# Optimization experiments

Hardware: AMD Instinct MI355X
Metric: run time of the kernel (lower is better)

## Reference

```python
import jax, jax.numpy as jnp
import numpy as np

R = 16
ALPHA = 32.0
SCALING = ALPHA / R


def setup_inputs() -> dict:
    key = jax.random.key(0)
    ks = jax.random.split(key, 6)
    B, T, C, O, E = 16, 1500, 1024, 1024, 8
    x = jax.random.normal(ks[0], (B, T, C), dtype=jnp.float32)
    # gate weights per batch element (e.g. softmax-like, but module accepts any)
    w = jax.random.uniform(ks[1], (B, E), dtype=jnp.float32)
    W_base = jax.random.normal(ks[2], (O, C), dtype=jnp.float32) * 0.02
    b_base = jax.random.normal(ks[3], (O,), dtype=jnp.float32) * 0.02
    As = jax.random.normal(ks[4], (E, R, C), dtype=jnp.float32) * 0.02
    Bs = jax.random.normal(ks[5], (E, O, R), dtype=jnp.float32) * 0.02
    return {"x": x, "w": w, "W_base": W_base, "b_base": b_base, "As": As, "Bs": Bs}


def reference(x, w, W_base, b_base, As, Bs):
    # base linear: (B,T,C) @ (C,O) + b
    out = jnp.einsum('btc,oc->bto', x, W_base) + b_base
    # per-expert low-rank: h[b,t,e,r] = x[b,t,:] @ A_e^T
    h = jnp.einsum('btc,erc->bter', x, As)          # (B,T,E,R)
    # y[b,t,e,o] = h @ B_e^T ; gate-weighted sum over experts
    lora = jnp.einsum('bter,eor,be->bto', h, Bs, w)  # (B,T,O)
    return out + lora * SCALING
```

## Files before the change

kernel.cpp:

```cpp
#include <hip/hip_runtime.h>
#include <stdint.h>
#include <stddef.h>


#define B_ 16
#define T_ 1500
#define C_ 1024
#define O_ 1024
#define E_ 8
#define R_ 16
#define ER 128
#define KK 1152
#define BT 24000
#define SCALING 2.0f

typedef __bf16 bf16x8 __attribute__((ext_vector_type(8)));
typedef float f32x4 __attribute__((ext_vector_type(4)));
typedef unsigned short u16;

__device__ inline u16 f2bf(float f) {
  union { float f; unsigned u; } v; v.f = f;
  unsigned u = v.u;
  u += 0x7fff + ((u >> 16) & 1);
  return (u16)(u >> 16);
}

#define GLL(gp, lp)                                                            \
  __builtin_amdgcn_global_load_lds(                                            \
      (const __attribute__((address_space(1))) void*)(gp),                     \
      (__attribute__((address_space(3))) void*)(lp), 16, 0, 0)

__global__ __launch_bounds__(256) void prep_w(const float* __restrict__ Wb,
                                              const float* __restrict__ Bs,
                                              const float* __restrict__ As,
                                              u16* __restrict__ wp,
                                              u16* __restrict__ ap) {
  int idx = blockIdx.x * 256 + threadIdx.x;
  if (idx < O_ * KK) {
    int o = idx / KK;
    int k = idx - o * KK;
    float v;
    if (k < C_) {
      v = Wb[o * C_ + k];
    } else {
      int j = k - C_;
      v = Bs[((j >> 4) * O_ + o) * R_ + (j & 15)];
    }
    wp[idx] = f2bf(v);
  } else {
    int a = idx - O_ * KK;
    ap[a] = f2bf(As[a]);
  }
}

__global__ __launch_bounds__(256) void cvt_h(const float* __restrict__ x,
                                             const u16* __restrict__ ab,
                                             const float* __restrict__ w,
                                             u16* __restrict__ xp) {
  const int mt = blockIdx.x;
  const int tid = threadIdx.x, lane = tid & 63, wv = tid >> 6;
  const int wrow = wv & 1, wcol = wv >> 1, l15 = lane & 15, quad = lane >> 4;
  const int kx = quad ^ (l15 & 3) ^ ((l15 >> 2) & 3);

  __shared__ u16 lA[64 * 40];
  __shared__ u16 lB[128 * 32];

  const size_t row0 = (size_t)mt * 64;

  f32x4 acc[2][4];
#pragma unroll
  for (int i = 0; i < 2; ++i)
#pragma unroll
    for (int j = 0; j < 4; ++j) acc[i][j] = (f32x4){0.f, 0.f, 0.f, 0.f};

  const int idx0 = tid, idx1 = 256 + tid;
  const int r0 = idx0 >> 2, kc0 = (idx0 & 3) ^ (r0 & 3) ^ ((r0 >> 2) & 3);
  const int r1 = idx1 >> 2, kc1 = (idx1 & 3) ^ (r1 & 3) ^ ((r1 >> 2) & 3);

  const int xr0 = tid >> 3;
  const int xr1 = xr0 + 32;
  const int xc = (tid & 7) * 4;

  for (int kt = 0; kt < C_ / 32; ++kt) {
    const int k0 = kt * 32;
    GLL(ab + r0 * C_ + k0 + kc0 * 8, &lB[idx0 * 8]);
    GLL(ab + r1 * C_ + k0 + kc1 * 8, &lB[idx1 * 8]);
    float4 v0 = *(const float4*)&x[(row0 + xr0) * C_ + k0 + xc];
    float4 v1 = *(const float4*)&x[(row0 + xr1) * C_ + k0 + xc];
    ushort4 o0, o1;
    o0.x = f2bf(v0.x); o0.y = f2bf(v0.y); o0.z = f2bf(v0.z); o0.w = f2bf(v0.w);
    o1.x = f2bf(v1.x); o1.y = f2bf(v1.y); o1.z = f2bf(v1.z); o1.w = f2bf(v1.w);
    *(ushort4*)&lA[xr0 * 40 + xc] = o0;
    *(ushort4*)&lA[xr1 * 40 + xc] = o1;
    *(ushort4*)&xp[(row0 + xr0) * KK + k0 + xc] = o0;
    *(ushort4*)&xp[(row0 + xr1) * KK + k0 + xc] = o1;
    __syncthreads();
    bf16x8 af[2], bfr[4];
#pragma unroll
    for (int i = 0; i < 2; ++i)
      af[i] = *(const bf16x8*)&lA[(wrow * 32 + i * 16 + l15) * 40 + quad * 8];
#pragma unroll
    for (int j = 0; j < 4; ++j)
      bfr[j] = *(const bf16x8*)&lB[(wcol * 64 + j * 16 + l15) * 32 + kx * 8];
#pragma unroll
    for (int i = 0; i < 2; ++i)
#pragma unroll
      for (int j = 0; j < 4; ++j)
        acc[i][j] = __builtin_amdgcn_mfma_f32_16x16x32_bf16(af[i], bfr[j], acc[i][j], 0, 0, 0);
    __syncthreads();
  }

#pragma unroll
  for (int j = 0; j < 4; ++j) {
    const int col = wcol * 64 + j * 16 + l15;
    const int e = wcol * 4 + j;
#pragma unroll
    for (int i = 0; i < 2; ++i) {
#pragma unroll
      for (int rr = 0; rr < 4; ++rr) {
        const int row = mt * 64 + wrow * 32 + i * 16 + quad * 4 + rr;
        const int b = row / T_;
        xp[(size_t)row * KK + C_ + col] = f2bf(acc[i][j][rr] * (SCALING * w[b * E_ + e]));
      }
    }
  }
}

__global__ __launch_bounds__(256) void main_gemm(const u16* __restrict__ xp,
                                                 const u16* __restrict__ wp,
                                                 const float* __restrict__ bb,
                                                 float* __restrict__ out) {
  const int id = blockIdx.x;
  const int mt = ((id >> 6) << 3) | (id & 7);
  const int nt = (id >> 3) & 7;
  if (mt >= 188) return;
  const int tid = threadIdx.x, lane = tid & 63, wv = tid >> 6;
  const int wrow = wv & 1, wcol = wv >> 1, l15 = lane & 15, quad = lane >> 4;
  const int kx = quad ^ (l15 & 3) ^ ((l15 >> 2) & 3);

  __shared__ u16 lA[128 * 32];
  __shared__ u16 lB[128 * 32];
  const u16* gA = xp + (size_t)mt * 128 * KK;
  const u16* gB = wp + (size_t)nt * 128 * KK;

  f32x4 acc[4][4];
#pragma unroll
  for (int i = 0; i < 4; ++i)
#pragma unroll
    for (int j = 0; j < 4; ++j) acc[i][j] = (f32x4){0.f, 0.f, 0.f, 0.f};

  const int idx0 = tid, idx1 = 256 + tid;
  const int r0 = idx0 >> 2, kc0 = (idx0 & 3) ^ (r0 & 3) ^ ((r0 >> 2) & 3);
  const int r1 = idx1 >> 2, kc1 = (idx1 & 3) ^ (r1 & 3) ^ ((r1 >> 2) & 3);

  for (int kt = 0; kt < KK / 32; ++kt) {
    const int k0 = kt * 32;
    GLL(gA + (size_t)r0 * KK + k0 + kc0 * 8, &lA[idx0 * 8]);
    GLL(gA + (size_t)r1 * KK + k0 + kc1 * 8, &lA[idx1 * 8]);
    GLL(gB + (size_t)r0 * KK + k0 + kc0 * 8, &lB[idx0 * 8]);
    GLL(gB + (size_t)r1 * KK + k0 + kc1 * 8, &lB[idx1 * 8]);
    __syncthreads();
    bf16x8 af[4], bfr[4];
#pragma unroll
    for (int i = 0; i < 4; ++i) {
      af[i] = *(const bf16x8*)&lA[(wrow * 64 + i * 16 + l15) * 32 + kx * 8];
      bfr[i] = *(const bf16x8*)&lB[(wcol * 64 + i * 16 + l15) * 32 + kx * 8];
    }
#pragma unroll
    for (int i = 0; i < 4; ++i)
#pragma unroll
      for (int j = 0; j < 4; ++j)
        acc[i][j] = __builtin_amdgcn_mfma_f32_16x16x32_bf16(af[i], bfr[j], acc[i][j], 0, 0, 0);
    __syncthreads();
  }

#pragma unroll
  for (int j = 0; j < 4; ++j) {
    const int col = nt * 128 + wcol * 64 + j * 16 + l15;
    const float bias = bb[col];
#pragma unroll
    for (int i = 0; i < 4; ++i) {
#pragma unroll
      for (int rr = 0; rr < 4; ++rr) {
        const int row = mt * 128 + wrow * 64 + i * 16 + quad * 4 + rr;
        if (row < BT) out[(size_t)row * O_ + col] = acc[i][j][rr] + bias;
      }
    }
  }
}

extern "C" void kernel_launch(void* const* d_in, const int* in_sizes, int n_in,
                              void* d_out, int out_size, void* d_ws, size_t ws_size,
                              hipStream_t stream) {
  const float* x = (const float*)d_in[0];
  const float* w = (const float*)d_in[1];
  const float* Wb = (const float*)d_in[2];
  const float* bb = (const float*)d_in[3];
  const float* As = (const float*)d_in[4];
  const float* Bs = (const float*)d_in[5];
  float* out = (float*)d_out;

  u16* xp = (u16*)d_ws;
  u16* wp = xp + (size_t)BT * KK;
  u16* ap = wp + (size_t)O_ * KK;

  prep_w<<<(O_ * KK + ER * C_) / 256, 256, 0, stream>>>(Wb, Bs, As, wp, ap);
  cvt_h<<<375, 256, 0, stream>>>(x, ap, w, xp);
  main_gemm<<<1536, 256, 0, stream>>>(xp, wp, bb, out);
}
```

Measured before the change: 299.0 us.

## Double K-tile depth to 64 and halve cvt_h row tile for more blocks

Both the conversion/low-rank kernel and the main GEMM now stage 64-wide K tiles in LDS with an 8-way XOR swizzle, halving the number of barrier pairs per K loop. cvt_h also processes 32 rows per block instead of 64, doubling its grid to 750 blocks for better occupancy of the memory-bound x conversion pass. The cost is larger LDS footprint per block (32KB in main_gemm), which may reduce concurrent blocks per CU.

```diff
diff --git a/kernel.cpp b/kernel.cpp
--- a/kernel.cpp
+++ b/kernel.cpp
@@ -60,53 +60,55 @@
   const int mt = blockIdx.x;
   const int tid = threadIdx.x, lane = tid & 63, wv = tid >> 6;
   const int wrow = wv & 1, wcol = wv >> 1, l15 = lane & 15, quad = lane >> 4;
-  const int kx = quad ^ (l15 & 3) ^ ((l15 >> 2) & 3);
-
-  __shared__ u16 lA[64 * 40];
-  __shared__ u16 lB[128 * 32];
-
-  const size_t row0 = (size_t)mt * 64;
-
-  f32x4 acc[2][4];
-#pragma unroll
-  for (int i = 0; i < 2; ++i)
-#pragma unroll
-    for (int j = 0; j < 4; ++j) acc[i][j] = (f32x4){0.f, 0.f, 0.f, 0.f};
-
-  const int idx0 = tid, idx1 = 256 + tid;
-  const int r0 = idx0 >> 2, kc0 = (idx0 & 3) ^ (r0 & 3) ^ ((r0 >> 2) & 3);
-  const int r1 = idx1 >> 2, kc1 = (idx1 & 3) ^ (r1 & 3) ^ ((r1 >> 2) & 3);
-
-  const int xr0 = tid >> 3;
-  const int xr1 = xr0 + 32;
+  const int s7 = l15 & 7;
+
+  __shared__ u16 lA[32 * 72];
+  __shared__ u16 lB[128 * 64];
+
+  const size_t row0 = (size_t)mt * 32;
+
+  f32x4 acc[4];
+#pragma unroll
+  for (int j = 0; j < 4; ++j) acc[j] = (f32x4){0.f, 0.f, 0.f, 0.f};
+
+  int brow[4], bko[4];
+#pragma unroll
+  for (int c = 0; c < 4; ++c) {
+    int idx = c * 256 + tid;
+    brow[c] = idx >> 3;
+    bko[c] = (((idx & 7) ^ (brow[c] & 7)) << 3);
+  }
+
+  const int xr = tid >> 3;
   const int xc = (tid & 7) * 4;
 
-  for (int kt = 0; kt < C_ / 32; ++kt) {
-    const int k0 = kt * 32;
-    GLL(ab + r0 * C_ + k0 + kc0 * 8, &lB[idx0 * 8]);
-    GLL(ab + r1 * C_ + k0 + kc1 * 8, &lB[idx1 * 8]);
-    float4 v0 = *(const float4*)&x[(row0 + xr0) * C_ + k0 + xc];
-    float4 v1 = *(const float4*)&x[(row0 + xr1) * C_ + k0 + xc];
+  for (int kt = 0; kt < C_ / 64; ++kt) {
+    const int k0 = kt * 64;
+#pragma unroll
+    for (int c = 0; c < 4; ++c)
+      GLL(ab + brow[c] * C_ + k0 + bko[c], &lB[(c * 256 + tid) * 8]);
+    float4 v0 = *(const float4*)&x[(row0 + xr) * C_ + k0 + xc];
+    float4 v1 = *(const float4*)&x[(row0 + xr) * C_ + k0 + 32 + xc];
     ushort4 o0, o1;
     o0.x = f2bf(v0.x); o0.y = f2bf(v0.y); o0.z = f2bf(v0.z); o0.w = f2bf(v0.w);
     o1.x = f2bf(v1.x); o1.y = f2bf(v1.y); o1.z = f2bf(v1.z); o1.w = f2bf(v1.w);
-    *(ushort4*)&lA[xr0 * 40 + xc] = o0;
-    *(ushort4*)&lA[xr1 * 40 + xc] = o1;
-    *(ushort4*)&xp[(row0 + xr0) * KK + k0 + xc] = o0;
-    *(ushort4*)&xp[(row0 + xr1) * KK + k0 + xc] = o1;
-    __syncthreads();
-    bf16x8 af[2], bfr[4];
-#pragma unroll
-    for (int i = 0; i < 2; ++i)
-      af[i] = *(const bf16x8*)&lA[(wrow * 32 + i * 16 + l15) * 40 + quad * 8];
-#pragma unroll
-    for (int j = 0; j < 4; ++j)
-      bfr[j] = *(const bf16x8*)&lB[(wcol * 64 + j * 16 + l15) * 32 + kx * 8];
-#pragma unroll
-    for (int i = 0; i < 2; ++i)
+    *(ushort4*)&lA[xr * 72 + xc] = o0;
+    *(ushort4*)&lA[xr * 72 + 32 + xc] = o1;
+    *(ushort4*)&xp[(row0 + xr) * KK + k0 + xc] = o0;
+    *(ushort4*)&xp[(row0 + xr) * KK + k0 + 32 + xc] = o1;
+    __syncthreads();
+#pragma unroll
+    for (int kk = 0; kk < 2; ++kk) {
+      bf16x8 af = *(const bf16x8*)&lA[(wrow * 16 + l15) * 72 + kk * 32 + quad * 8];
+      bf16x8 bfr[4];
 #pragma unroll
       for (int j = 0; j < 4; ++j)
-        acc[i][j] = __builtin_amdgcn_mfma_f32_16x16x32_bf16(af[i], bfr[j], acc[i][j], 0, 0, 0);
+        bfr[j] = *(const bf16x8*)&lB[(wcol * 64 + j * 16 + l15) * 64 +
+                                     (((kk * 4 + quad) ^ s7) << 3)];
+#pragma unroll
+      for (int j = 0; j < 4; ++j)
+        acc[j] = __builtin_amdgcn_mfma_f32_16x16x32_bf16(af, bfr[j], acc[j], 0, 0, 0);
+    }
     __syncthreads();
   }
 
@@ -115,13 +117,10 @@
     const int col = wcol * 64 + j * 16 + l15;
     const int e = wcol * 4 + j;
 #pragma unroll
-    for (int i = 0; i < 2; ++i) {
-#pragma unroll
-      for (int rr = 0; rr < 4; ++rr) {
-        const int row = mt * 64 + wrow * 32 + i * 16 + quad * 4 + rr;
-        const int b = row / T_;
-        xp[(size_t)row * KK + C_ + col] = f2bf(acc[i][j][rr] * (SCALING * w[b * E_ + e]));
-      }
+    for (int rr = 0; rr < 4; ++rr) {
+      const int row = mt * 32 + wrow * 16 + quad * 4 + rr;
+      const int b = row / T_;
+      xp[(size_t)row * KK + C_ + col] = f2bf(acc[j][rr] * (SCALING * w[b * E_ + e]));
     }
   }
 }
@@ -136,10 +135,10 @@
   if (mt >= 188) return;
   const int tid = threadIdx.x, lane = tid & 63, wv = tid >> 6;
   const int wrow = wv & 1, wcol = wv >> 1, l15 = lane & 15, quad = lane >> 4;
-  const int kx = quad ^ (l15 & 3) ^ ((l15 >> 2) & 3);
-
-  __shared__ u16 lA[128 * 32];
-  __shared__ u16 lB[128 * 32];
+  const int s7 = l15 & 7;
+
+  __shared__ u16 lA[128 * 64];
+  __shared__ u16 lB[128 * 64];
   const u16* gA = xp + (size_t)mt * 128 * KK;
   const u16* gB = wp + (size_t)nt * 128 * KK;
 
@@ -149,28 +148,38 @@
 #pragma unroll
     for (int j = 0; j < 4; ++j) acc[i][j] = (f32x4){0.f, 0.f, 0.f, 0.f};
 
-  const int idx0 = tid, idx1 = 256 + tid;
-  const int r0 = idx0 >> 2, kc0 = (idx0 & 3) ^ (r0 & 3) ^ ((r0 >> 2) & 3);
-  const int r1 = idx1 >> 2, kc1 = (idx1 & 3) ^ (r1 & 3) ^ ((r1 >> 2) & 3);
-
-  for (int kt = 0; kt < KK / 32; ++kt) {
-    const int k0 = kt * 32;
-    GLL(gA + (size_t)r0 * KK + k0 + kc0 * 8, &lA[idx0 * 8]);
-    GLL(gA + (size_t)r1 * KK + k0 + kc1 * 8, &lA[idx1 * 8]);
-    GLL(gB + (size_t)r0 * KK + k0 + kc0 * 8, &lB[idx0 * 8]);
-    GLL(gB + (size_t)r1 * KK + k0 + kc1 * 8, &lB[idx1 * 8]);
-    __syncthreads();
-    bf16x8 af[4], bfr[4];
-#pragma unroll
-    for (int i = 0; i < 4; ++i) {
-      af[i] = *(const bf16x8*)&lA[(wrow * 64 + i * 16 + l15) * 32 + kx * 8];
-      bfr[i] = *(const bf16x8*)&lB[(wcol * 64 + i * 16 + l15) * 32 + kx * 8];
-    }
-#pragma unroll
-    for (int i = 0; i < 4; ++i)
-#pragma unroll
-      for (int j = 0; j < 4; ++j)
-        acc[i][j] = __builtin_amdgcn_mfma_f32_16x16x32_bf16(af[i], bfr[j], acc[i][j], 0, 0, 0);
+  int srow[4], sko[4];
+#pragma unroll
+  for (int c = 0; c < 4; ++c) {
+    int idx = c * 256 + tid;
+    srow[c] = idx >> 3;
+    sko[c] = (((idx & 7) ^ (srow[c] & 7)) << 3);
+  }
+
+  for (int kt = 0; kt < KK / 64; ++kt) {
+    const int k0 = kt * 64;
+#pragma unroll
+    for (int c = 0; c < 4; ++c)
+      GLL(gA + (size_t)srow[c] * KK + k0 + sko[c], &lA[(c * 256 + tid) * 8]);
+#pragma unroll
+    for (int c = 0; c < 4; ++c)
+      GLL(gB + (size_t)srow[c] * KK + k0 + sko[c], &lB[(c * 256 + tid) * 8]);
+    __syncthreads();
+#pragma unroll
+    for (int kk = 0; kk < 2; ++kk) {
+      bf16x8 af[4], bfr[4];
+#pragma unroll
+      for (int i = 0; i < 4; ++i) {
+        const int ko = (((kk * 4 + quad) ^ s7) << 3);
+        af[i] = *(const bf16x8*)&lA[(wrow * 64 + i * 16 + l15) * 64 + ko];
+        bfr[i] = *(const bf16x8*)&lB[(wcol * 64 + i * 16 + l15) * 64 + ko];
+      }
+#pragma unroll
+      for (int i = 0; i < 4; ++i)
+#pragma unroll
+        for (int j = 0; j < 4; ++j)
+          acc[i][j] = __builtin_amdgcn_mfma_f32_16x16x32_bf16(af[i], bfr[j], acc[i][j], 0, 0, 0);
+    }
     __syncthreads();
   }
 
@@ -205,6 +214,6 @@
   u16* ap = wp + (size_t)O_ * KK;
 
   prep_w<<<(O_ * KK + ER * C_) / 256, 256, 0, stream>>>(Wb, Bs, As, wp, ap);
-  cvt_h<<<375, 256, 0, stream>>>(x, ap, w, xp);
+  cvt_h<<<750, 256, 0, stream>>>(x, ap, w, xp);
   main_gemm<<<1536, 256, 0, stream>>>(xp, wp, bb, out);
 }
```

Result: faster. 285.7 us (-4.4%).

## Split x conversion into a streaming kernel and retile the LoRA-h GEMM

Applied to the files above, without the earlier changes.

The fused convert-plus-h-GEMM kernel becomes two kernels. The first is a fully parallel fp32-to-bf16 conversion of x into the workspace. The second is an h GEMM that reads the bf16 x with direct global-to-LDS loads, uses a 64-wide K tile and an XOR swizzle. The goal is to stop the fp32 load and convert work from serialising with the MFMA loop across only 375 blocks. The cost is an extra launch and a second read of x in bf16 from the workspace.

```diff
diff --git a/kernel.cpp b/kernel.cpp
--- a/kernel.cpp
+++ b/kernel.cpp
@@ -17,6 +17,7 @@
 typedef __bf16 bf16x8 __attribute__((ext_vector_type(8)));
 typedef float f32x4 __attribute__((ext_vector_type(4)));
 typedef unsigned short u16;
+typedef u16 u16x8 __attribute__((ext_vector_type(8)));
 
 __device__ inline u16 f2bf(float f) {
   union { float f; unsigned u; } v; v.f = f;
@@ -53,19 +54,36 @@
   }
 }
 
-__global__ __launch_bounds__(256) void cvt_h(const float* __restrict__ x,
-                                             const u16* __restrict__ ab,
-                                             const float* __restrict__ w,
-                                             u16* __restrict__ xp) {
+__global__ __launch_bounds__(256) void cvt(const float* __restrict__ x,
+                                           u16* __restrict__ xp) {
+  const int t0 = blockIdx.x * 256 + threadIdx.x;
+#pragma unroll
+  for (int u = 0; u < 6; ++u) {
+    const int chunk = u * 512000 + t0;
+    const int row = chunk >> 7;
+    const int cc = (chunk & 127) * 8;
+    const float4 v0 = *(const float4*)&x[(size_t)row * C_ + cc];
+    const float4 v1 = *(const float4*)&x[(size_t)row * C_ + cc + 4];
+    u16x8 o;
+    o[0] = f2bf(v0.x); o[1] = f2bf(v0.y); o[2] = f2bf(v0.z); o[3] = f2bf(v0.w);
+    o[4] = f2bf(v1.x); o[5] = f2bf(v1.y); o[6] = f2bf(v1.z); o[7] = f2bf(v1.w);
+    *(u16x8*)&xp[(size_t)row * KK + cc] = o;
+  }
+}
+
+__global__ __launch_bounds__(256) void h_gemm(const u16* __restrict__ xp,
+                                              const u16* __restrict__ ab,
+                                              const float* __restrict__ w,
+                                              u16* __restrict__ xpo) {
   const int mt = blockIdx.x;
   const int tid = threadIdx.x, lane = tid & 63, wv = tid >> 6;
   const int wrow = wv & 1, wcol = wv >> 1, l15 = lane & 15, quad = lane >> 4;
-  const int kx = quad ^ (l15 & 3) ^ ((l15 >> 2) & 3);
-
-  __shared__ u16 lA[64 * 40];
-  __shared__ u16 lB[128 * 32];
-
-  const size_t row0 = (size_t)mt * 64;
+  const int s7 = l15 & 7;
+
+  __shared__ u16 lA[64 * 64];
+  __shared__ u16 lB[128 * 64];
+
+  const u16* gA = xp + (size_t)mt * 64 * KK;
 
   f32x4 acc[2][4];
 #pragma unroll
@@ -73,40 +91,45 @@
 #pragma unroll
     for (int j = 0; j < 4; ++j) acc[i][j] = (f32x4){0.f, 0.f, 0.f, 0.f};
 
-  const int idx0 = tid, idx1 = 256 + tid;
-  const int r0 = idx0 >> 2, kc0 = (idx0 & 3) ^ (r0 & 3) ^ ((r0 >> 2) & 3);
-  const int r1 = idx1 >> 2, kc1 = (idx1 & 3) ^ (r1 & 3) ^ ((r1 >> 2) & 3);
-
-  const int xr0 = tid >> 3;
-  const int xr1 = xr0 + 32;
-  const int xc = (tid & 7) * 4;
-
-  for (int kt = 0; kt < C_ / 32; ++kt) {
-    const int k0 = kt * 32;
-    GLL(ab + r0 * C_ + k0 + kc0 * 8, &lB[idx0 * 8]);
-    GLL(ab + r1 * C_ + k0 + kc1 * 8, &lB[idx1 * 8]);
-    float4 v0 = *(const float4*)&x[(row0 + xr0) * C_ + k0 + xc];
-    float4 v1 = *(const float4*)&x[(row0 + xr1) * C_ + k0 + xc];
-    ushort4 o0, o1;
-    o0.x = f2bf(v0.x); o0.y = f2bf(v0.y); o0.z = f2bf(v0.z); o0.w = f2bf(v0.w);
-    o1.x = f2bf(v1.x); o1.y = f2bf(v1.y); o1.z = f2bf(v1.z); o1.w = f2bf(v1.w);
-    *(ushort4*)&lA[xr0 * 40 + xc] = o0;
-    *(ushort4*)&lA[xr1 * 40 + xc] = o1;
-    *(ushort4*)&xp[(row0 + xr0) * KK + k0 + xc] = o0;
-    *(ushort4*)&xp[(row0 + xr1) * KK + k0 + xc] = o1;
-    __syncthreads();
-    bf16x8 af[2], bfr[4];
-#pragma unroll
-    for (int i = 0; i < 2; ++i)
-      af[i] = *(const bf16x8*)&lA[(wrow * 32 + i * 16 + l15) * 40 + quad * 8];
-#pragma unroll
-    for (int j = 0; j < 4; ++j)
-      bfr[j] = *(const bf16x8*)&lB[(wcol * 64 + j * 16 + l15) * 32 + kx * 8];
-#pragma unroll
-    for (int i = 0; i < 2; ++i)
+  int arow[2], ako[2], brow[4], bko[4];
+#pragma unroll
+  for (int c = 0; c < 2; ++c) {
+    int idx = c * 256 + tid;
+    arow[c] = idx >> 3;
+    ako[c] = (((idx & 7) ^ (arow[c] & 7)) << 3);
+  }
+#pragma unroll
+  for (int c = 0; c < 4; ++c) {
+    int idx = c * 256 + tid;
+    brow[c] = idx >> 3;
+    bko[c] = (((idx & 7) ^ (brow[c] & 7)) << 3);
+  }
+
+  for (int kt = 0; kt < C_ / 64; ++kt) {
+    const int k0 = kt * 64;
+#pragma unroll
+    for (int c = 0; c < 2; ++c)
+      GLL(gA + (size_t)arow[c] * KK + k0 + ako[c], &lA[(c * 256 + tid) * 8]);
+#pragma unroll
+    for (int c = 0; c < 4; ++c)
+      GLL(ab + brow[c] * C_ + k0 + bko[c], &lB[(c * 256 + tid) * 8]);
+    __syncthreads();
+#pragma unroll
+    for (int kk = 0; kk < 2; ++kk) {
+      const int ko = (((kk * 4 + quad) ^ s7) << 3);
+      bf16x8 af[2], bfr[4];
+#pragma unroll
+      for (int i = 0; i < 2; ++i)
+        af[i] = *(const bf16x8*)&lA[(wrow * 32 + i * 16 + l15) * 64 + ko];
 #pragma unroll
       for (int j = 0; j < 4; ++j)
-        acc[i][j] = __builtin_amdgcn_mfma_f32_16x16x32_bf16(af[i], bfr[j], acc[i][j], 0, 0, 0);
+        bfr[j] = *(const bf16x8*)&lB[(wcol * 64 + j * 16 + l15) * 64 + ko];
+#pragma unroll
+      for (int i = 0; i < 2; ++i)
+#pragma unroll
+        for (int j = 0; j < 4; ++j)
+          acc[i][j] = __builtin_amdgcn_mfma_f32_16x16x32_bf16(af[i], bfr[j], acc[i][j], 0, 0, 0);
+    }
     __syncthreads();
   }
 
@@ -120,7 +143,7 @@
       for (int rr = 0; rr < 4; ++rr) {
         const int row = mt * 64 + wrow * 32 + i * 16 + quad * 4 + rr;
         const int b = row / T_;
-        xp[(size_t)row * KK + C_ + col] = f2bf(acc[i][j][rr] * (SCALING * w[b * E_ + e]));
+        xpo[(size_t)row * KK + C_ + col] = f2bf(acc[i][j][rr] * (SCALING * w[b * E_ + e]));
       }
     }
   }
@@ -205,6 +228,7 @@
   u16* ap = wp + (size_t)O_ * KK;
 
   prep_w<<<(O_ * KK + ER * C_) / 256, 256, 0, stream>>>(Wb, Bs, As, wp, ap);
-  cvt_h<<<375, 256, 0, stream>>>(x, ap, w, xp);
+  cvt<<<2000, 256, 0, stream>>>(x, xp);
+  h_gemm<<<375, 256, 0, stream>>>(xp, ap, w, xp);
   main_gemm<<<1536, 256, 0, stream>>>(xp, wp, bb, out);
 }
```

Result: faster. 292.4 us (-2.2%).
